# Optimization experiments

Hardware: AMD Instinct MI355X
Metric: run time of the kernel (lower is better)

## Reference

```python
import jax, jax.numpy as jnp
import numpy as np

EPS = 1e-4  # clamp from module default (0.0001, 1 - 0.0001)


def setup_inputs() -> dict:
    key = jax.random.key(0)
    k1, k2, k3 = jax.random.split(key, 3)
    B, T, C, K = 16, 4096, 512, 3
    x = jax.random.normal(k1, (B, T, C), dtype=jnp.float32)
    # logit_alpha initialized as logit of (0.8, 0.9, 0.98) tiled across channels
    init_alphas = jnp.array([0.8, 0.9, 0.98], dtype=jnp.float32)
    logit_alpha = jnp.broadcast_to(
        (jnp.log(init_alphas) - jnp.log1p(-init_alphas))[:, None], (K, C)
    ).astype(jnp.float32)
    # add small noise so gradients are non-degenerate
    logit_alpha = logit_alpha + 0.01 * jax.random.normal(k2, (K, C), dtype=jnp.float32)
    mix_logits = 0.1 * jax.random.normal(k3, (C, K), dtype=jnp.float32)
    return {"x": x, "logit_alpha": logit_alpha, "mix_logits": mix_logits}


def reference(x, logit_alpha, mix_logits):
    # x: [B,T,C]; logit_alpha: [K,C]; mix_logits: [C,K]
    B, T, C = x.shape
    K = logit_alpha.shape[0]
    a = jnp.clip(jax.nn.sigmoid(logit_alpha), EPS, 1.0 - EPS)  # [K,C]
    b = 1.0 - a

    y0 = jnp.broadcast_to(x[:, 0, None, :], (B, K, C))  # t=0: y = x0 for all K

    def step(y_prev, xt):
        # y_prev: [B,K,C], xt: [B,C]
        y = a * y_prev + b * xt[:, None, :]
        return y, y

    xs = jnp.swapaxes(x[:, 1:, :], 0, 1)  # [T-1,B,C]
    _, ys = jax.lax.scan(step, y0, xs)  # [T-1,B,K,C]
    yk = jnp.concatenate([y0[None], ys], axis=0)  # [T,B,K,C]

    mix = jax.nn.softmax(mix_logits, axis=-1)  # [C,K]
    trend = jnp.einsum('tbkc,ck->tbc', yk, mix)  # [T,B,C]
    return jnp.swapaxes(trend, 0, 1)  # [B,T,C]
```

## Files before the change

kernel.cpp:

```cpp
#include <hip/hip_runtime.h>

#define DEV_INLINE __device__ __forceinline__

constexpr int B = 16, T = 4096, C = 512, K = 3;
constexpr int NC = 64;
constexpr int L  = T / NC;
constexpr int C4 = C / 4;
constexpr float EPS = 1e-4f;


typedef float f4v __attribute__((ext_vector_type(4)));

DEV_INLINE float4 f4mul(float4 a, float4 b) {
  return make_float4(a.x * b.x, a.y * b.y, a.z * b.z, a.w * b.w);
}
DEV_INLINE float4 f4fma(float4 a, float4 b, float4 c) {
  return make_float4(fmaf(a.x, b.x, c.x), fmaf(a.y, b.y, c.y),
                     fmaf(a.z, b.z, c.z), fmaf(a.w, b.w, c.w));
}
DEV_INLINE float4 f4onesub(float4 a) {
  return make_float4(1.f - a.x, 1.f - a.y, 1.f - a.z, 1.f - a.w);
}

DEV_INLINE float sig_clamp(float v) {
  float a = 1.0f / (1.0f + __expf(-v));
  return fminf(fmaxf(a, EPS), 1.0f - EPS);
}
DEV_INLINE float4 sig4(float4 v) {
  return make_float4(sig_clamp(v.x), sig_clamp(v.y), sig_clamp(v.z), sig_clamp(v.w));
}

DEV_INLINE void sm3(float l0, float l1, float l2, float& o0, float& o1, float& o2) {
  float mx = fmaxf(l0, fmaxf(l1, l2));
  float e0 = __expf(l0 - mx), e1 = __expf(l1 - mx), e2 = __expf(l2 - mx);
  float inv = 1.0f / (e0 + e1 + e2);
  o0 = e0 * inv; o1 = e1 * inv; o2 = e2 * inv;
}

DEV_INLINE void nt_store(float4* p, float4 v) {
  f4v t; t.x = v.x; t.y = v.y; t.z = v.z; t.w = v.w;
  __builtin_nontemporal_store(t, reinterpret_cast<f4v*>(p));
}

__global__ __launch_bounds__(128) void ema_k1(const float* __restrict__ x,
                                              const float* __restrict__ logit_alpha,
                                              float* __restrict__ carry_f) {
  const int c4 = threadIdx.x;
  const int bi = blockIdx.x;
  const int i  = bi & (NC - 1);

  const float4* la = (const float4*)logit_alpha;
  const float4 a0 = sig4(la[0 * C4 + c4]);
  const float4 a1 = sig4(la[1 * C4 + c4]);
  const float4 a2 = sig4(la[2 * C4 + c4]);
  const float4 b0 = f4onesub(a0), b1 = f4onesub(a1), b2 = f4onesub(a2);

  const float4* xb = (const float4*)x + (size_t)bi * L * C4 + c4;

  float4 y0, y1, y2;
  int jstart;
  if (i == 0) {
    float4 x0 = xb[0];
    y0 = x0; y1 = x0; y2 = x0;
    jstart = 1;
  } else {
    y0 = make_float4(0.f, 0.f, 0.f, 0.f);
    y1 = y0; y2 = y0;
    jstart = 0;
  }

  #pragma unroll 4
  for (int j = jstart; j < L; ++j) {
    float4 xv = xb[(size_t)j * C4];
    y0 = f4fma(a0, y0, f4mul(b0, xv));
    y1 = f4fma(a1, y1, f4mul(b1, xv));
    y2 = f4fma(a2, y2, f4mul(b2, xv));
  }

  float4* carry = (float4*)carry_f;
  const size_t cb = (size_t)bi * (K * C4) + c4;
  carry[cb + 0 * C4] = y0;
  carry[cb + 1 * C4] = y1;
  carry[cb + 2 * C4] = y2;
}

__global__ __launch_bounds__(128) void ema_k2(const float* __restrict__ x,
                                              const float* __restrict__ logit_alpha,
                                              const float* __restrict__ mix_logits,
                                              const float* __restrict__ carry_f,
                                              float* __restrict__ out) {
  const int c4 = threadIdx.x;
  const int bi = blockIdx.x;
  const int i  = bi & (NC - 1);
  const int b  = bi >> 6;

  const float4* la = (const float4*)logit_alpha;
  const float4 a0 = sig4(la[0 * C4 + c4]);
  const float4 a1 = sig4(la[1 * C4 + c4]);
  const float4 a2 = sig4(la[2 * C4 + c4]);
  const float4 b0 = f4onesub(a0), b1 = f4onesub(a1), b2 = f4onesub(a2);

  const float4* ml = (const float4*)mix_logits;
  const float4 q0 = ml[3 * c4 + 0];
  const float4 q1 = ml[3 * c4 + 1];
  const float4 q2 = ml[3 * c4 + 2];
  float4 m0, m1, m2;
  sm3(q0.x, q0.y, q0.z, m0.x, m1.x, m2.x);
  sm3(q0.w, q1.x, q1.y, m0.y, m1.y, m2.y);
  sm3(q1.z, q1.w, q2.x, m0.z, m1.z, m2.z);
  sm3(q2.y, q2.z, q2.w, m0.w, m1.w, m2.w);

  const float4* xb = (const float4*)x + (size_t)bi * L * C4 + c4;
  float4*       ob = (float4*)out     + (size_t)bi * L * C4 + c4;

  float4 y0, y1, y2;
  int jstart;
  if (i == 0) {
    float4 x0 = xb[0];
    y0 = x0; y1 = x0; y2 = x0;
    nt_store(&ob[0], f4fma(m0, y0, f4fma(m1, y1, f4mul(m2, y2))));
    jstart = 1;
  } else {
    float4 A0 = a0, A1 = a1, A2 = a2;
    #pragma unroll
    for (int s = 0; s < 6; ++s) { A0 = f4mul(A0, A0); A1 = f4mul(A1, A1); A2 = f4mul(A2, A2); }

    const size_t stride = (size_t)K * C4;
    const float4* cb = (const float4*)carry_f + (size_t)b * NC * stride + c4;
    y0 = cb[0 * C4];
    y1 = cb[1 * C4];
    y2 = cb[2 * C4];
    #pragma unroll 4
    for (int j = 1; j < i; ++j) {
      const float4* cj = cb + (size_t)j * stride;
      y0 = f4fma(A0, y0, cj[0 * C4]);
      y1 = f4fma(A1, y1, cj[1 * C4]);
      y2 = f4fma(A2, y2, cj[2 * C4]);
    }
    jstart = 0;
  }

  #pragma unroll 4
  for (int j = jstart; j < L; ++j) {
    float4 xv = xb[(size_t)j * C4];
    y0 = f4fma(a0, y0, f4mul(b0, xv));
    y1 = f4fma(a1, y1, f4mul(b1, xv));
    y2 = f4fma(a2, y2, f4mul(b2, xv));
    nt_store(&ob[(size_t)j * C4], f4fma(m0, y0, f4fma(m1, y1, f4mul(m2, y2))));
  }
}

extern "C" void kernel_launch(void* const* d_in, const int* in_sizes, int n_in,
                              void* d_out, int out_size, void* d_ws, size_t ws_size,
                              hipStream_t stream) {
  const float* x           = (const float*)d_in[0];
  const float* logit_alpha = (const float*)d_in[1];
  const float* mix_logits  = (const float*)d_in[2];
  float* out = (float*)d_out;
  float* ws  = (float*)d_ws;

  ema_k1<<<B * NC, 128, 0, stream>>>(x, logit_alpha, ws);
  ema_k2<<<B * NC, 128, 0, stream>>>(x, logit_alpha, mix_logits, ws, out);
}
```

Baseline: 265.5 us.

## Write local scan output in pass one and add carry correction in pass two

The first kernel now writes the mixed output of the zero-initialised local scan while streaming x, so x is read once instead of twice. The second kernel no longer reads x. It reads the output back and adds a carry correction computed as powers of alpha times the mixed incoming carry. This turns the old x read plus out write in pass two into an out read plus out write, and drops the nontemporal stores, so its benefit depends on how much of the output written in pass one is still in cache.

```diff
diff --git a/kernel.cpp b/kernel.cpp
--- a/kernel.cpp
+++ b/kernel.cpp
@@ -13,6 +13,9 @@
 
 DEV_INLINE float4 f4mul(float4 a, float4 b) {
   return make_float4(a.x * b.x, a.y * b.y, a.z * b.z, a.w * b.w);
+}
+DEV_INLINE float4 f4add(float4 a, float4 b) {
+  return make_float4(a.x + b.x, a.y + b.y, a.z + b.z, a.w + b.w);
 }
 DEV_INLINE float4 f4fma(float4 a, float4 b, float4 c) {
   return make_float4(fmaf(a.x, b.x, c.x), fmaf(a.y, b.y, c.y),
@@ -37,14 +40,28 @@
   o0 = e0 * inv; o1 = e1 * inv; o2 = e2 * inv;
 }
 
-DEV_INLINE void nt_store(float4* p, float4 v) {
-  f4v t; t.x = v.x; t.y = v.y; t.z = v.z; t.w = v.w;
-  __builtin_nontemporal_store(t, reinterpret_cast<f4v*>(p));
+DEV_INLINE float4 nt_load(const float4* p) {
+  f4v t = __builtin_nontemporal_load(reinterpret_cast<const f4v*>(p));
+  float4 r; r.x = t.x; r.y = t.y; r.z = t.z; r.w = t.w; return r;
+}
+
+DEV_INLINE void mix4(const float* __restrict__ mix_logits, int c4,
+                     float4& m0, float4& m1, float4& m2) {
+  const float4* ml = (const float4*)mix_logits;
+  const float4 q0 = ml[3 * c4 + 0];
+  const float4 q1 = ml[3 * c4 + 1];
+  const float4 q2 = ml[3 * c4 + 2];
+  sm3(q0.x, q0.y, q0.z, m0.x, m1.x, m2.x);
+  sm3(q0.w, q1.x, q1.y, m0.y, m1.y, m2.y);
+  sm3(q1.z, q1.w, q2.x, m0.z, m1.z, m2.z);
+  sm3(q2.y, q2.z, q2.w, m0.w, m1.w, m2.w);
 }
 
 __global__ __launch_bounds__(128) void ema_k1(const float* __restrict__ x,
                                               const float* __restrict__ logit_alpha,
-                                              float* __restrict__ carry_f) {
+                                              const float* __restrict__ mix_logits,
+                                              float* __restrict__ carry_f,
+                                              float* __restrict__ out) {
   const int c4 = threadIdx.x;
   const int bi = blockIdx.x;
   const int i  = bi & (NC - 1);
@@ -55,13 +72,18 @@
   const float4 a2 = sig4(la[2 * C4 + c4]);
   const float4 b0 = f4onesub(a0), b1 = f4onesub(a1), b2 = f4onesub(a2);
 
+  float4 m0, m1, m2;
+  mix4(mix_logits, c4, m0, m1, m2);
+
   const float4* xb = (const float4*)x + (size_t)bi * L * C4 + c4;
+  float4*       ob = (float4*)out     + (size_t)bi * L * C4 + c4;
 
   float4 y0, y1, y2;
   int jstart;
   if (i == 0) {
-    float4 x0 = xb[0];
+    float4 x0 = nt_load(&xb[0]);
     y0 = x0; y1 = x0; y2 = x0;
+    ob[0] = f4fma(m0, y0, f4fma(m1, y1, f4mul(m2, y2)));
     jstart = 1;
   } else {
     y0 = make_float4(0.f, 0.f, 0.f, 0.f);
@@ -71,10 +93,11 @@
 
   #pragma unroll 4
   for (int j = jstart; j < L; ++j) {
-    float4 xv = xb[(size_t)j * C4];
+    float4 xv = nt_load(&xb[(size_t)j * C4]);
     y0 = f4fma(a0, y0, f4mul(b0, xv));
     y1 = f4fma(a1, y1, f4mul(b1, xv));
     y2 = f4fma(a2, y2, f4mul(b2, xv));
+    ob[(size_t)j * C4] = f4fma(m0, y0, f4fma(m1, y1, f4mul(m2, y2)));
   }
 
   float4* carry = (float4*)carry_f;
@@ -84,69 +107,55 @@
   carry[cb + 2 * C4] = y2;
 }
 
-__global__ __launch_bounds__(128) void ema_k2(const float* __restrict__ x,
-                                              const float* __restrict__ logit_alpha,
+__global__ __launch_bounds__(128) void ema_k2(const float* __restrict__ logit_alpha,
                                               const float* __restrict__ mix_logits,
                                               const float* __restrict__ carry_f,
                                               float* __restrict__ out) {
-  const int c4 = threadIdx.x;
-  const int bi = blockIdx.x;
-  const int i  = bi & (NC - 1);
-  const int b  = bi >> 6;
+  const int c4  = threadIdx.x;
+  const int blk = blockIdx.x;
+  const int b   = blk / (NC - 1);
+  const int i   = blk - b * (NC - 1) + 1;
 
   const float4* la = (const float4*)logit_alpha;
   const float4 a0 = sig4(la[0 * C4 + c4]);
   const float4 a1 = sig4(la[1 * C4 + c4]);
   const float4 a2 = sig4(la[2 * C4 + c4]);
-  const float4 b0 = f4onesub(a0), b1 = f4onesub(a1), b2 = f4onesub(a2);
 
-  const float4* ml = (const float4*)mix_logits;
-  const float4 q0 = ml[3 * c4 + 0];
-  const float4 q1 = ml[3 * c4 + 1];
-  const float4 q2 = ml[3 * c4 + 2];
   float4 m0, m1, m2;
-  sm3(q0.x, q0.y, q0.z, m0.x, m1.x, m2.x);
-  sm3(q0.w, q1.x, q1.y, m0.y, m1.y, m2.y);
-  sm3(q1.z, q1.w, q2.x, m0.z, m1.z, m2.z);
-  sm3(q2.y, q2.z, q2.w, m0.w, m1.w, m2.w);
+  mix4(mix_logits, c4, m0, m1, m2);
 
-  const float4* xb = (const float4*)x + (size_t)bi * L * C4 + c4;
-  float4*       ob = (float4*)out     + (size_t)bi * L * C4 + c4;
+  float4 A0 = a0, A1 = a1, A2 = a2;
+  #pragma unroll
+  for (int s = 0; s < 6; ++s) { A0 = f4mul(A0, A0); A1 = f4mul(A1, A1); A2 = f4mul(A2, A2); }
 
-  float4 y0, y1, y2;
-  int jstart;
-  if (i == 0) {
-    float4 x0 = xb[0];
-    y0 = x0; y1 = x0; y2 = x0;
-    nt_store(&ob[0], f4fma(m0, y0, f4fma(m1, y1, f4mul(m2, y2))));
-    jstart = 1;
-  } else {
-    float4 A0 = a0, A1 = a1, A2 = a2;
-    #pragma unroll
-    for (int s = 0; s < 6; ++s) { A0 = f4mul(A0, A0); A1 = f4mul(A1, A1); A2 = f4mul(A2, A2); }
-
-    const size_t stride = (size_t)K * C4;
-    const float4* cb = (const float4*)carry_f + (size_t)b * NC * stride + c4;
-    y0 = cb[0 * C4];
-    y1 = cb[1 * C4];
-    y2 = cb[2 * C4];
-    #pragma unroll 4
-    for (int j = 1; j < i; ++j) {
-      const float4* cj = cb + (size_t)j * stride;
-      y0 = f4fma(A0, y0, cj[0 * C4]);
-      y1 = f4fma(A1, y1, cj[1 * C4]);
-      y2 = f4fma(A2, y2, cj[2 * C4]);
-    }
-    jstart = 0;
+  const size_t stride = (size_t)K * C4;
+  const float4* cb = (const float4*)carry_f + (size_t)b * NC * stride + c4;
+  float4 E0 = cb[0 * C4];
+  float4 E1 = cb[1 * C4];
+  float4 E2 = cb[2 * C4];
+  #pragma unroll 4
+  for (int j = 1; j < i; ++j) {
+    const float4* cj = cb + (size_t)j * stride;
+    E0 = f4fma(A0, E0, cj[0 * C4]);
+    E1 = f4fma(A1, E1, cj[1 * C4]);
+    E2 = f4fma(A2, E2, cj[2 * C4]);
   }
 
+  const float4 g0 = f4mul(m0, E0);
+  const float4 g1 = f4mul(m1, E1);
+  const float4 g2 = f4mul(m2, E2);
+  float4 p0 = a0, p1 = a1, p2 = a2;
+
+  float4* ob = (float4*)out + (size_t)(b * NC + i) * L * C4 + c4;
+
   #pragma unroll 4
-  for (int j = jstart; j < L; ++j) {
-    float4 xv = xb[(size_t)j * C4];
-    y0 = f4fma(a0, y0, f4mul(b0, xv));
-    y1 = f4fma(a1, y1, f4mul(b1, xv));
-    y2 = f4fma(a2, y2, f4mul(b2, xv));
-    nt_store(&ob[(size_t)j * C4], f4fma(m0, y0, f4fma(m1, y1, f4mul(m2, y2))));
+  for (int j = 0; j < L; ++j) {
+    float4 corr = f4fma(p0, g0, f4fma(p1, g1, f4mul(p2, g2)));
+    float4 o = ob[(size_t)j * C4];
+    ob[(size_t)j * C4] = f4add(o, corr);
+    p0 = f4mul(p0, a0);
+    p1 = f4mul(p1, a1);
+    p2 = f4mul(p2, a2);
   }
 }
 
@@ -159,6 +168,6 @@
   float* out = (float*)d_out;
   float* ws  = (float*)d_ws;
 
-  ema_k1<<<B * NC, 128, 0, stream>>>(x, logit_alpha, ws);
-  ema_k2<<<B * NC, 128, 0, stream>>>(x, logit_alpha, mix_logits, ws, out);
+  ema_k1<<<B * NC, 128, 0, stream>>>(x, logit_alpha, mix_logits, ws, out);
+  ema_k2<<<B * (NC - 1), 128, 0, stream>>>(logit_alpha, mix_logits, ws, out);
 }
```

Result: slower. 273.3 us (+2.9%).
